# Performance work log

Measured on AMD Instinct MI355X. Metric: run time of the kernel, lower is better.

The kernel has to match this reference:

```python
import jax, jax.numpy as jnp
import numpy as np

EPS = 1e-12

def _fuzzy_laplacian_weights(theta, src, dst, num_nodes):
    # Continuous edge directions: forward (src->dst) strength cos^2(theta),
    # backward (dst->src) strength sin^2(theta); each symmetrically normalized
    # by its own weighted in/out degrees.
    c = jnp.cos(theta); s = jnp.sin(theta)
    w_f = c * c
    w_b = s * s
    def norm(w):
        deg_out = jax.ops.segment_sum(w, src, num_segments=num_nodes)
        deg_in = jax.ops.segment_sum(w, dst, num_segments=num_nodes)
        return w * jax.lax.rsqrt(deg_out[src] * deg_in[dst] + EPS)
    return norm(w_f), norm(w_b)

def setup_inputs() -> dict:
    key = jax.random.key(0)
    ks = jax.random.split(key, 12)
    N, E, D, H, O, L = 50000, 800000, 128, 128, 64, 2
    x = jax.random.normal(ks[0], (N, D), dtype=jnp.float32)
    edge_index = jax.random.randint(ks[1], (2, E), 0, N, dtype=jnp.int64)
    theta = jax.random.uniform(ks[2], (E,), dtype=jnp.float32) * (np.pi / 2)
    sc = 0.05
    Ws2d = jax.random.normal(ks[3], (L, D, H), dtype=jnp.float32) * sc
    Wd2s = jax.random.normal(ks[4], (L, D, H), dtype=jnp.float32) * sc
    Wself = jax.random.normal(ks[5], (L, D, H), dtype=jnp.float32) * sc
    bs2d = jnp.zeros((L, H), jnp.float32)
    bd2s = jnp.zeros((L, H), jnp.float32)
    bself = jnp.zeros((L, H), jnp.float32)
    W_ro = jax.random.normal(ks[6], (H, O), dtype=jnp.float32) * sc
    b_ro = jnp.zeros((O,), jnp.float32)
    return {"x": x, "edge_index": edge_index, "theta": theta,
            "Ws2d": Ws2d, "Wd2s": Wd2s, "Wself": Wself,
            "bs2d": bs2d, "bd2s": bd2s, "bself": bself,
            "W_ro": W_ro, "b_ro": b_ro}

def reference(x, edge_index, theta, Ws2d, Wd2s, Wself, bs2d, bd2s, bself, W_ro, b_ro):
    N = x.shape[0]
    src, dst = edge_index[0], edge_index[1]
    w_f, w_b = _fuzzy_laplacian_weights(theta, src, dst, N)
    L = Ws2d.shape[0]
    for i in range(L):
        xj = x[src]                               # [E, D] gather
        a_s2d = jax.ops.segment_sum(xj * w_f[:, None], dst, num_segments=N)
        a_d2s = jax.ops.segment_sum(xj * w_b[:, None], dst, num_segments=N)
        h = (a_s2d @ Ws2d[i] + bs2d[i]
             + a_d2s @ Wd2s[i] + bd2s[i]
             + x @ Wself[i] + bself[i])
        if i != L - 1:
            h = jax.nn.relu(h)
            h = h / jnp.maximum(jnp.linalg.norm(h, axis=1, keepdims=True), EPS)
        x = h
    return x @ W_ro + b_ro
```

## Files before the change

kernel.cpp:

```cpp
#include <hip/hip_runtime.h>
#include <math.h>


constexpr int D = 128;
typedef unsigned long long u64;
typedef __attribute__((ext_vector_type(8))) short bf16x8;
typedef __attribute__((ext_vector_type(4))) float f32x4;

__device__ __forceinline__ u64 pack_wc(float f) {
    return (1ULL << 44) | (u64)(f * 16777216.0f + 0.5f);
}
__device__ __forceinline__ void unpack_wc(u64 p, float& sumf, float& cnt) {
    cnt  = (float)(unsigned)(p >> 44);
    sumf = (float)(p & ((1ULL << 44) - 1)) * (1.0f / 16777216.0f);
}

__device__ __forceinline__ void split_bf16(float x, short& hi, short& lo) {
    unsigned xb = __float_as_uint(x);
    hi = (short)(xb >> 16);
    float h = __uint_as_float(xb & 0xffff0000u);
    lo = (short)(__float_as_uint(x - h) >> 16);
}

__global__ __launch_bounds__(256) void edge_wdeg_kernel(
    const float* __restrict__ theta, const int* __restrict__ src, const int* __restrict__ dst,
    u64* __restrict__ packed_out, u64* __restrict__ packed_in, int E)
{
    int e = blockIdx.x * 256 + threadIdx.x;
    if (e >= E) return;
    float c = cosf(theta[e]);
    u64 p = pack_wc(c * c);
    atomicAdd(&packed_out[src[e]], p);
    atomicAdd(&packed_in[dst[e]], p);
}

__global__ __launch_bounds__(1024) void scan_kernel(
    const u64* __restrict__ packed_in, int* __restrict__ startv, int N)
{
    __shared__ int wsum[16];
    __shared__ int carry;
    if (threadIdx.x == 0) carry = 0;
    __syncthreads();
    const int lane = threadIdx.x & 63, wid = threadIdx.x >> 6;
    for (int base = 0; base < N; base += 1024) {
        int i = base + threadIdx.x;
        int v = (i < N) ? (int)(packed_in[i] >> 44) : 0;
        int x = v;
        #pragma unroll
        for (int d = 1; d < 64; d <<= 1) {
            int t = __shfl_up(x, d);
            if (lane >= d) x += t;
        }
        if (lane == 63) wsum[wid] = x;
        __syncthreads();
        if (wid == 0) {
            int s = (lane < 16) ? wsum[lane] : 0;
            #pragma unroll
            for (int d = 1; d < 16; d <<= 1) {
                int t = __shfl_up(s, d);
                if (lane >= d) s += t;
            }
            if (lane < 16) wsum[lane] = s;
        }
        __syncthreads();
        int woff = (wid == 0) ? 0 : wsum[wid - 1];
        if (i < N) startv[i] = carry + woff + x - v;
        __syncthreads();
        if (threadIdx.x == 1023) carry += wsum[15];
        __syncthreads();
    }
}

__global__ __launch_bounds__(256) void scatter_kernel(
    const float* __restrict__ theta, const int* __restrict__ src, const int* __restrict__ dst,
    const u64* __restrict__ packed_out, const u64* __restrict__ packed_in,
    int* __restrict__ startv, int4* __restrict__ s_edge, int E)
{
    int e = blockIdx.x * 256 + threadIdx.x;
    if (e >= E) return;
    int u = src[e], v = dst[e];
    float s, c;
    sincosf(theta[e], &s, &c);
    float f = c * c, b = s * s;
    float fo, co, fi, ci;
    unpack_wc(packed_out[u], fo, co);
    unpack_wc(packed_in[v], fi, ci);
    float bo = co - fo, bi = ci - fi;
    f *= rsqrtf(fo * fi + 1e-12f);
    b *= rsqrtf(bo * bi + 1e-12f);
    int pos = atomicAdd(&startv[v], 1);
    s_edge[pos] = make_int4(u, __float_as_int(f), __float_as_int(b), 0);
}

__global__ __launch_bounds__(256) void wpack_kernel(
    const float* __restrict__ W1, const float* __restrict__ W2, const float* __restrict__ W3,
    short* __restrict__ wp)
{
    int idx = blockIdx.x * 256 + threadIdx.x;
    if (idx >= 3 * 8 * 4 * 64) return;
    int lane = idx & 63;
    int t = (idx >> 6) & 3;
    int c = (idx >> 8) & 7;
    int m = idx >> 11;
    const float* W = (m == 0) ? W1 : ((m == 1) ? W2 : W3);
    int col  = c * 16 + (lane & 15);
    int row0 = t * 32 + (lane >> 4) * 8;
    short hi[8], lo[8];
    #pragma unroll
    for (int j = 0; j < 8; ++j)
        split_bf16(W[(size_t)(row0 + j) * 128 + col], hi[j], lo[j]);
    short* dst = wp + (size_t)idx * 16;
    #pragma unroll
    for (int j = 0; j < 8; ++j) { dst[j] = hi[j]; dst[8 + j] = lo[j]; }
}

__global__ __launch_bounds__(256) void agg_x_kernel(
    const int* __restrict__ endv, const int4* __restrict__ s_edge,
    const float* __restrict__ x,
    float* __restrict__ a1, float* __restrict__ a2, int N)
{
    int v = blockIdx.x * 4 + (threadIdx.x >> 6);
    if (v >= N) return;
    int lane = threadIdx.x & 63;
    int beg = (v == 0) ? 0 : endv[v - 1];
    int end = endv[v];
    float2 s1 = make_float2(0.f, 0.f), s2 = make_float2(0.f, 0.f);
    int e = beg;
    for (; e + 1 < end; e += 2) {
        int4 E0 = s_edge[e], E1 = s_edge[e + 1];
        float f0 = __int_as_float(E0.y), b0 = __int_as_float(E0.z);
        float f1 = __int_as_float(E1.y), b1 = __int_as_float(E1.z);
        float2 x0 = reinterpret_cast<const float2*>(x + (size_t)E0.x * 128)[lane];
        float2 x1 = reinterpret_cast<const float2*>(x + (size_t)E1.x * 128)[lane];
        s1.x = fmaf(f0, x0.x, s1.x); s1.y = fmaf(f0, x0.y, s1.y);
        s2.x = fmaf(b0, x0.x, s2.x); s2.y = fmaf(b0, x0.y, s2.y);
        s1.x = fmaf(f1, x1.x, s1.x); s1.y = fmaf(f1, x1.y, s1.y);
        s2.x = fmaf(b1, x1.x, s2.x); s2.y = fmaf(b1, x1.y, s2.y);
    }
    if (e < end) {
        int4 E0 = s_edge[e];
        float f0 = __int_as_float(E0.y), b0 = __int_as_float(E0.z);
        float2 x0 = reinterpret_cast<const float2*>(x + (size_t)E0.x * 128)[lane];
        s1.x = fmaf(f0, x0.x, s1.x); s1.y = fmaf(f0, x0.y, s1.y);
        s2.x = fmaf(b0, x0.x, s2.x); s2.y = fmaf(b0, x0.y, s2.y);
    }
    reinterpret_cast<float2*>(a1 + (size_t)v * 128)[lane] = s1;
    reinterpret_cast<float2*>(a2 + (size_t)v * 128)[lane] = s2;
}

__global__ __launch_bounds__(256, 2) void matmul_fused_kernel(
    const float* __restrict__ a1, const float* __restrict__ a2,
    const float* __restrict__ xin, const short* __restrict__ wp,
    const float* __restrict__ b1, const float* __restrict__ b2, const float* __restrict__ b3,
    float* __restrict__ h, int N)
{
    const int lane = threadIdx.x & 63, wid = threadIdx.x >> 6;
    const int row0 = blockIdx.x * 64 + wid * 16;

    int arow = row0 + (lane & 15);
    if (arow >= N) arow = N - 1;
    const size_t roff = (size_t)arow * 128 + (lane >> 4) * 8;
    const float* srcs[3] = {a1, a2, xin};
    bf16x8 ahi[3][4], alo[3][4];
    #pragma unroll
    for (int m = 0; m < 3; ++m) {
        const float* rp = srcs[m] + roff;
        #pragma unroll
        for (int t = 0; t < 4; ++t) {
            float4 v0 = *reinterpret_cast<const float4*>(rp + t * 32);
            float4 v1 = *reinterpret_cast<const float4*>(rp + t * 32 + 4);
            float f[8] = {v0.x, v0.y, v0.z, v0.w, v1.x, v1.y, v1.z, v1.w};
            #pragma unroll
            for (int j = 0; j < 8; ++j) {
                short hh, ll;
                split_bf16(f[j], hh, ll);
                ahi[m][t][j] = hh;
                alo[m][t][j] = ll;
            }
        }
    }

    const int colbase = lane & 15;
    const int rbase = row0 + (lane >> 4) * 4;
    #pragma unroll
    for (int c = 0; c < 8; ++c) {
        f32x4 a = {0.f, 0.f, 0.f, 0.f};
        #pragma unroll
        for (int t = 0; t < 4; ++t) {
            #pragma unroll
            for (int m = 0; m < 3; ++m) {
                const short* bp = wp + (size_t)((m * 8 + c) * 4 + t) * 1024 + lane * 16;
                bf16x8 bhi = *reinterpret_cast<const bf16x8*>(bp);
                bf16x8 blo = *reinterpret_cast<const bf16x8*>(bp + 8);
                a = __builtin_amdgcn_mfma_f32_16x16x32_bf16(ahi[m][t], bhi, a, 0, 0, 0);
                a = __builtin_amdgcn_mfma_f32_16x16x32_bf16(ahi[m][t], blo, a, 0, 0, 0);
                a = __builtin_amdgcn_mfma_f32_16x16x32_bf16(alo[m][t], bhi, a, 0, 0, 0);
            }
        }
        int col = c * 16 + colbase;
        float bias = b1[col] + b2[col] + b3[col];
        a[0] += bias; a[1] += bias; a[2] += bias; a[3] += bias;
        #pragma unroll
        for (int r = 0; r < 4; ++r) {
            int rr = rbase + r;
            if (rr < N) h[(size_t)rr * 128 + col] = a[r];
        }
    }
}

__global__ __launch_bounds__(256) void relu_rownorm_kernel(float* __restrict__ h, int N)
{
    int row = blockIdx.x * 4 + (threadIdx.x >> 6);
    if (row >= N) return;
    int lane = threadIdx.x & 63;
    float2* p = reinterpret_cast<float2*>(h + (size_t)row * 128) + lane;
    float2 v = *p;
    v.x = fmaxf(v.x, 0.f);
    v.y = fmaxf(v.y, 0.f);
    float ss = v.x * v.x + v.y * v.y;
    #pragma unroll
    for (int m = 1; m < 64; m <<= 1) ss += __shfl_xor(ss, m);
    float sc = 1.f / fmaxf(sqrtf(ss), 1e-12f);
    v.x *= sc; v.y *= sc;
    *p = v;
}

__global__ __launch_bounds__(256) void readout_kernel(
    const float* __restrict__ x, const float* __restrict__ W,
    const float* __restrict__ bias, float* __restrict__ out, int N)
{
    __shared__ float xs[64 * 132];
    const int tid = threadIdx.x;
    const int row0 = blockIdx.x * 64;
    #pragma unroll
    for (int j = 0; j < 8; ++j) {
        int g4 = tid + j * 256;
        int r = g4 >> 5, c4 = g4 & 31;
        float4 v = make_float4(0.f, 0.f, 0.f, 0.f);
        if (row0 + r < N)
            v = reinterpret_cast<const float4*>(x + (size_t)(row0 + r) * D)[c4];
        *reinterpret_cast<float4*>(xs + r * 132 + c4 * 4) = v;
    }
    __syncthreads();

    const int cg = tid & 15;
    const int rg = tid >> 4;
    float a[4][4];
    #pragma unroll
    for (int i = 0; i < 4; ++i)
        #pragma unroll
        for (int j = 0; j < 4; ++j) a[i][j] = 0.f;

    for (int k = 0; k < 128; k += 4) {
        float4 w0 = *reinterpret_cast<const float4*>(W + (size_t)(k + 0) * 64 + cg * 4);
        float4 w1 = *reinterpret_cast<const float4*>(W + (size_t)(k + 1) * 64 + cg * 4);
        float4 w2 = *reinterpret_cast<const float4*>(W + (size_t)(k + 2) * 64 + cg * 4);
        float4 w3 = *reinterpret_cast<const float4*>(W + (size_t)(k + 3) * 64 + cg * 4);
        #pragma unroll
        for (int i = 0; i < 4; ++i) {
            float4 xv = *reinterpret_cast<const float4*>(xs + (rg * 4 + i) * 132 + k);
            a[i][0] += xv.x * w0.x + xv.y * w1.x + xv.z * w2.x + xv.w * w3.x;
            a[i][1] += xv.x * w0.y + xv.y * w1.y + xv.z * w2.y + xv.w * w3.y;
            a[i][2] += xv.x * w0.z + xv.y * w1.z + xv.z * w2.z + xv.w * w3.z;
            a[i][3] += xv.x * w0.w + xv.y * w1.w + xv.z * w2.w + xv.w * w3.w;
        }
    }
    #pragma unroll
    for (int i = 0; i < 4; ++i) {
        int r = row0 + rg * 4 + i;
        if (r < N) {
            float4 o = make_float4(a[i][0] + bias[cg * 4 + 0], a[i][1] + bias[cg * 4 + 1],
                                   a[i][2] + bias[cg * 4 + 2], a[i][3] + bias[cg * 4 + 3]);
            *reinterpret_cast<float4*>(out + (size_t)r * 64 + cg * 4) = o;
        }
    }
}

extern "C" void kernel_launch(void* const* d_in, const int* in_sizes, int n_in,
                              void* d_out, int out_size, void* d_ws, size_t ws_size,
                              hipStream_t stream)
{
    const float* x     = (const float*)d_in[0];
    const int*   ei    = (const int*)d_in[1];
    const float* theta = (const float*)d_in[2];
    const float* Ws2d  = (const float*)d_in[3];
    const float* Wd2s  = (const float*)d_in[4];
    const float* Wself = (const float*)d_in[5];
    const float* bs2d  = (const float*)d_in[6];
    const float* bd2s  = (const float*)d_in[7];
    const float* bself = (const float*)d_in[8];
    const float* W_ro  = (const float*)d_in[9];
    const float* b_ro  = (const float*)d_in[10];
    float* out = (float*)d_out;

    const int N = in_sizes[0] / D;
    const int E = in_sizes[2];
    const int L = in_sizes[3] / (D * D);

    const int* src = ei;
    const int* dst = ei + E;

    u64*  packed_out = (u64*)d_ws;
    u64*  packed_in  = packed_out + N;
    int*  startv     = (int*)(packed_in + N);
    int4* s_edge     = (int4*)(startv + N);
    short* wpack     = (short*)(s_edge + E);
    float* a1   = (float*)(wpack + (size_t)L * 98304);
    float* a2   = a1 + (size_t)N * D;
    float* accA = a2 + (size_t)N * D;
    float* accB = accA + (size_t)N * D;

    hipMemsetAsync(packed_out, 0, (size_t)2 * N * sizeof(u64), stream);
    edge_wdeg_kernel<<<(E + 255) / 256, 256, 0, stream>>>(
        theta, src, dst, packed_out, packed_in, E);
    scan_kernel<<<1, 1024, 0, stream>>>(packed_in, startv, N);
    scatter_kernel<<<(E + 255) / 256, 256, 0, stream>>>(
        theta, src, dst, packed_out, packed_in, startv, s_edge, E);
    for (int i = 0; i < L; ++i)
        wpack_kernel<<<(6144 + 255) / 256, 256, 0, stream>>>(
            Ws2d + (size_t)i * D * D, Wd2s + (size_t)i * D * D, Wself + (size_t)i * D * D,
            wpack + (size_t)i * 98304);

    const float* xin = x;
    float* accs[2] = {accA, accB};
    for (int i = 0; i < L; ++i) {
        float* acc = accs[i & 1];
        agg_x_kernel<<<(N + 3) / 4, 256, 0, stream>>>(
            startv, s_edge, xin, a1, a2, N);
        matmul_fused_kernel<<<(N + 63) / 64, 256, 0, stream>>>(
            a1, a2, xin, wpack + (size_t)i * 98304,
            bs2d + (size_t)i * D, bd2s + (size_t)i * D, bself + (size_t)i * D,
            acc, N);
        if (i != L - 1)
            relu_rownorm_kernel<<<(N + 3) / 4, 256, 0, stream>>>(acc, N);
        xin = acc;
    }
    readout_kernel<<<(N + 63) / 64, 256, 0, stream>>>(xin, W_ro, b_ro, out, N);
}
```

Measured before the change: 537.4 us.

## Fuse relu-rownorm into matmul, MFMA readout, unroll aggregation, two-per-thread scan

The ReLU and row L2-normalisation are folded into the matmul epilogue. The 128-column row norm is reduced across the 16 lanes that hold a row, which removes a separate kernel's full read and write of the hidden matrix. The scalar-FMA readout kernel becomes an MFMA kernel using a bf16 hi/lo split of W_ro, packed once by a new small kernel. The aggregation loop is unrolled to four edges to keep more gathers in flight, and the scan handles two elements per thread to halve its iterations. The cost is more register pressure in the matmul, which now keeps all eight output tiles live.

```diff
diff --git a/kernel.cpp b/kernel.cpp
--- a/kernel.cpp
+++ b/kernel.cpp
@@ -42,10 +42,13 @@
     if (threadIdx.x == 0) carry = 0;
     __syncthreads();
     const int lane = threadIdx.x & 63, wid = threadIdx.x >> 6;
-    for (int base = 0; base < N; base += 1024) {
-        int i = base + threadIdx.x;
-        int v = (i < N) ? (int)(packed_in[i] >> 44) : 0;
-        int x = v;
+    for (int base = 0; base < N; base += 2048) {
+        int i0 = base + threadIdx.x * 2;
+        int i1 = i0 + 1;
+        int v0 = (i0 < N) ? (int)(packed_in[i0] >> 44) : 0;
+        int v1 = (i1 < N) ? (int)(packed_in[i1] >> 44) : 0;
+        int pair = v0 + v1;
+        int x = pair;
         #pragma unroll
         for (int d = 1; d < 64; d <<= 1) {
             int t = __shfl_up(x, d);
@@ -64,7 +67,9 @@
         }
         __syncthreads();
         int woff = (wid == 0) ? 0 : wsum[wid - 1];
-        if (i < N) startv[i] = carry + woff + x - v;
+        int excl = carry + woff + x - pair;
+        if (i0 < N) startv[i0] = excl;
+        if (i1 < N) startv[i1] = excl + v0;
         __syncthreads();
         if (threadIdx.x == 1023) carry += wsum[15];
         __syncthreads();
@@ -114,6 +119,25 @@
     for (int j = 0; j < 8; ++j) { dst[j] = hi[j]; dst[8 + j] = lo[j]; }
 }
 
+__global__ __launch_bounds__(256) void wpack_ro_kernel(
+    const float* __restrict__ W, short* __restrict__ wp)
+{
+    int idx = blockIdx.x * 256 + threadIdx.x;
+    if (idx >= 4 * 4 * 64) return;
+    int lane = idx & 63;
+    int t = (idx >> 6) & 3;
+    int c = idx >> 8;
+    int col  = c * 16 + (lane & 15);
+    int row0 = t * 32 + (lane >> 4) * 8;
+    short hi[8], lo[8];
+    #pragma unroll
+    for (int j = 0; j < 8; ++j)
+        split_bf16(W[(size_t)(row0 + j) * 64 + col], hi[j], lo[j]);
+    short* dst = wp + (size_t)idx * 16;
+    #pragma unroll
+    for (int j = 0; j < 8; ++j) { dst[j] = hi[j]; dst[8 + j] = lo[j]; }
+}
+
 __global__ __launch_bounds__(256) void agg_x_kernel(
     const int* __restrict__ endv, const int4* __restrict__ s_edge,
     const float* __restrict__ x,
@@ -126,18 +150,26 @@
     int end = endv[v];
     float2 s1 = make_float2(0.f, 0.f), s2 = make_float2(0.f, 0.f);
     int e = beg;
-    for (; e + 1 < end; e += 2) {
-        int4 E0 = s_edge[e], E1 = s_edge[e + 1];
+    for (; e + 3 < end; e += 4) {
+        int4 E0 = s_edge[e], E1 = s_edge[e + 1], E2 = s_edge[e + 2], E3 = s_edge[e + 3];
+        float2 x0 = reinterpret_cast<const float2*>(x + (size_t)E0.x * 128)[lane];
+        float2 x1 = reinterpret_cast<const float2*>(x + (size_t)E1.x * 128)[lane];
+        float2 x2 = reinterpret_cast<const float2*>(x + (size_t)E2.x * 128)[lane];
+        float2 x3 = reinterpret_cast<const float2*>(x + (size_t)E3.x * 128)[lane];
         float f0 = __int_as_float(E0.y), b0 = __int_as_float(E0.z);
         float f1 = __int_as_float(E1.y), b1 = __int_as_float(E1.z);
-        float2 x0 = reinterpret_cast<const float2*>(x + (size_t)E0.x * 128)[lane];
-        float2 x1 = reinterpret_cast<const float2*>(x + (size_t)E1.x * 128)[lane];
+        float f2 = __int_as_float(E2.y), b2 = __int_as_float(E2.z);
+        float f3 = __int_as_float(E3.y), b3 = __int_as_float(E3.z);
         s1.x = fmaf(f0, x0.x, s1.x); s1.y = fmaf(f0, x0.y, s1.y);
         s2.x = fmaf(b0, x0.x, s2.x); s2.y = fmaf(b0, x0.y, s2.y);
         s1.x = fmaf(f1, x1.x, s1.x); s1.y = fmaf(f1, x1.y, s1.y);
         s2.x = fmaf(b1, x1.x, s2.x); s2.y = fmaf(b1, x1.y, s2.y);
-    }
-    if (e < end) {
+        s1.x = fmaf(f2, x2.x, s1.x); s1.y = fmaf(f2, x2.y, s1.y);
+        s2.x = fmaf(b2, x2.x, s2.x); s2.y = fmaf(b2, x2.y, s2.y);
+        s1.x = fmaf(f3, x3.x, s1.x); s1.y = fmaf(f3, x3.y, s1.y);
+        s2.x = fmaf(b3, x3.x, s2.x); s2.y = fmaf(b3, x3.y, s2.y);
+    }
+    for (; e < end; ++e) {
         int4 E0 = s_edge[e];
         float f0 = __int_as_float(E0.y), b0 = __int_as_float(E0.z);
         float2 x0 = reinterpret_cast<const float2*>(x + (size_t)E0.x * 128)[lane];
@@ -148,6 +180,7 @@
     reinterpret_cast<float2*>(a2 + (size_t)v * 128)[lane] = s2;
 }
 
+template <bool NORM>
 __global__ __launch_bounds__(256, 2) void matmul_fused_kernel(
     const float* __restrict__ a1, const float* __restrict__ a2,
     const float* __restrict__ xin, const short* __restrict__ wp,
@@ -182,6 +215,7 @@
 
     const int colbase = lane & 15;
     const int rbase = row0 + (lane >> 4) * 4;
+    f32x4 acc[8];
     #pragma unroll
     for (int c = 0; c < 8; ++c) {
         f32x4 a = {0.f, 0.f, 0.f, 0.f};
@@ -200,78 +234,97 @@
         int col = c * 16 + colbase;
         float bias = b1[col] + b2[col] + b3[col];
         a[0] += bias; a[1] += bias; a[2] += bias; a[3] += bias;
+        acc[c] = a;
+    }
+
+    if (NORM) {
+        #pragma unroll
+        for (int c = 0; c < 8; ++c) {
+            acc[c][0] = fmaxf(acc[c][0], 0.f);
+            acc[c][1] = fmaxf(acc[c][1], 0.f);
+            acc[c][2] = fmaxf(acc[c][2], 0.f);
+            acc[c][3] = fmaxf(acc[c][3], 0.f);
+        }
+        float ss[4] = {0.f, 0.f, 0.f, 0.f};
+        #pragma unroll
+        for (int c = 0; c < 8; ++c) {
+            ss[0] = fmaf(acc[c][0], acc[c][0], ss[0]);
+            ss[1] = fmaf(acc[c][1], acc[c][1], ss[1]);
+            ss[2] = fmaf(acc[c][2], acc[c][2], ss[2]);
+            ss[3] = fmaf(acc[c][3], acc[c][3], ss[3]);
+        }
+        #pragma unroll
+        for (int r = 0; r < 4; ++r) {
+            #pragma unroll
+            for (int m = 1; m < 16; m <<= 1) ss[r] += __shfl_xor(ss[r], m);
+        }
+        float sc[4];
+        #pragma unroll
+        for (int r = 0; r < 4; ++r) sc[r] = 1.f / fmaxf(sqrtf(ss[r]), 1e-12f);
+        #pragma unroll
+        for (int c = 0; c < 8; ++c) {
+            acc[c][0] *= sc[0]; acc[c][1] *= sc[1];
+            acc[c][2] *= sc[2]; acc[c][3] *= sc[3];
+        }
+    }
+
+    #pragma unroll
+    for (int c = 0; c < 8; ++c) {
+        int col = c * 16 + colbase;
         #pragma unroll
         for (int r = 0; r < 4; ++r) {
             int rr = rbase + r;
-            if (rr < N) h[(size_t)rr * 128 + col] = a[r];
-        }
-    }
-}
-
-__global__ __launch_bounds__(256) void relu_rownorm_kernel(float* __restrict__ h, int N)
-{
-    int row = blockIdx.x * 4 + (threadIdx.x >> 6);
-    if (row >= N) return;
-    int lane = threadIdx.x & 63;
-    float2* p = reinterpret_cast<float2*>(h + (size_t)row * 128) + lane;
-    float2 v = *p;
-    v.x = fmaxf(v.x, 0.f);
-    v.y = fmaxf(v.y, 0.f);
-    float ss = v.x * v.x + v.y * v.y;
-    #pragma unroll
-    for (int m = 1; m < 64; m <<= 1) ss += __shfl_xor(ss, m);
-    float sc = 1.f / fmaxf(sqrtf(ss), 1e-12f);
-    v.x *= sc; v.y *= sc;
-    *p = v;
-}
-
-__global__ __launch_bounds__(256) void readout_kernel(
-    const float* __restrict__ x, const float* __restrict__ W,
+            if (rr < N) h[(size_t)rr * 128 + col] = acc[c][r];
+        }
+    }
+}
+
+__global__ __launch_bounds__(256, 2) void readout_mfma_kernel(
+    const float* __restrict__ xin, const short* __restrict__ wp,
     const float* __restrict__ bias, float* __restrict__ out, int N)
 {
-    __shared__ float xs[64 * 132];
-    const int tid = threadIdx.x;
-    const int row0 = blockIdx.x * 64;
-    #pragma unroll
-    for (int j = 0; j < 8; ++j) {
-        int g4 = tid + j * 256;
-        int r = g4 >> 5, c4 = g4 & 31;
-        float4 v = make_float4(0.f, 0.f, 0.f, 0.f);
-        if (row0 + r < N)
-            v = reinterpret_cast<const float4*>(x + (size_t)(row0 + r) * D)[c4];
-        *reinterpret_cast<float4*>(xs + r * 132 + c4 * 4) = v;
-    }
-    __syncthreads();
-
-    const int cg = tid & 15;
-    const int rg = tid >> 4;
-    float a[4][4];
-    #pragma unroll
-    for (int i = 0; i < 4; ++i)
-        #pragma unroll
-        for (int j = 0; j < 4; ++j) a[i][j] = 0.f;
-
-    for (int k = 0; k < 128; k += 4) {
-        float4 w0 = *reinterpret_cast<const float4*>(W + (size_t)(k + 0) * 64 + cg * 4);
-        float4 w1 = *reinterpret_cast<const float4*>(W + (size_t)(k + 1) * 64 + cg * 4);
-        float4 w2 = *reinterpret_cast<const float4*>(W + (size_t)(k + 2) * 64 + cg * 4);
-        float4 w3 = *reinterpret_cast<const float4*>(W + (size_t)(k + 3) * 64 + cg * 4);
-        #pragma unroll
-        for (int i = 0; i < 4; ++i) {
-            float4 xv = *reinterpret_cast<const float4*>(xs + (rg * 4 + i) * 132 + k);
-            a[i][0] += xv.x * w0.x + xv.y * w1.x + xv.z * w2.x + xv.w * w3.x;
-            a[i][1] += xv.x * w0.y + xv.y * w1.y + xv.z * w2.y + xv.w * w3.y;
-            a[i][2] += xv.x * w0.z + xv.y * w1.z + xv.z * w2.z + xv.w * w3.z;
-            a[i][3] += xv.x * w0.w + xv.y * w1.w + xv.z * w2.w + xv.w * w3.w;
-        }
-    }
-    #pragma unroll
-    for (int i = 0; i < 4; ++i) {
-        int r = row0 + rg * 4 + i;
-        if (r < N) {
-            float4 o = make_float4(a[i][0] + bias[cg * 4 + 0], a[i][1] + bias[cg * 4 + 1],
-                                   a[i][2] + bias[cg * 4 + 2], a[i][3] + bias[cg * 4 + 3]);
-            *reinterpret_cast<float4*>(out + (size_t)r * 64 + cg * 4) = o;
+    const int lane = threadIdx.x & 63, wid = threadIdx.x >> 6;
+    const int row0 = blockIdx.x * 64 + wid * 16;
+
+    int arow = row0 + (lane & 15);
+    if (arow >= N) arow = N - 1;
+    const float* rp = xin + (size_t)arow * 128 + (lane >> 4) * 8;
+    bf16x8 ahi[4], alo[4];
+    #pragma unroll
+    for (int t = 0; t < 4; ++t) {
+        float4 v0 = *reinterpret_cast<const float4*>(rp + t * 32);
+        float4 v1 = *reinterpret_cast<const float4*>(rp + t * 32 + 4);
+        float f[8] = {v0.x, v0.y, v0.z, v0.w, v1.x, v1.y, v1.z, v1.w};
+        #pragma unroll
+        for (int j = 0; j < 8; ++j) {
+            short hh, ll;
+            split_bf16(f[j], hh, ll);
+            ahi[t][j] = hh;
+            alo[t][j] = ll;
+        }
+    }
+
+    const int colbase = lane & 15;
+    const int rbase = row0 + (lane >> 4) * 4;
+    #pragma unroll
+    for (int c = 0; c < 4; ++c) {
+        f32x4 a = {0.f, 0.f, 0.f, 0.f};
+        #pragma unroll
+        for (int t = 0; t < 4; ++t) {
+            const short* bp = wp + (size_t)((c * 4 + t) * 64 + lane) * 16;
+            bf16x8 bhi = *reinterpret_cast<const bf16x8*>(bp);
+            bf16x8 blo = *reinterpret_cast<const bf16x8*>(bp + 8);
+            a = __builtin_amdgcn_mfma_f32_16x16x32_bf16(ahi[t], bhi, a, 0, 0, 0);
+            a = __builtin_amdgcn_mfma_f32_16x16x32_bf16(ahi[t], blo, a, 0, 0, 0);
+            a = __builtin_amdgcn_mfma_f32_16x16x32_bf16(alo[t], bhi, a, 0, 0, 0);
+        }
+        int col = c * 16 + colbase;
+        float bv = bias[col];
+        a[0] += bv; a[1] += bv; a[2] += bv; a[3] += bv;
+        #pragma unroll
+        for (int r = 0; r < 4; ++r) {
+            int rr = rbase + r;
+            if (rr < N) out[(size_t)rr * 64 + col] = a[r];
         }
     }
 }
@@ -305,7 +358,8 @@
     int*  startv     = (int*)(packed_in + N);
     int4* s_edge     = (int4*)(startv + N);
     short* wpack     = (short*)(s_edge + E);
-    float* a1   = (float*)(wpack + (size_t)L * 98304);
+    short* wpack_ro  = wpack + (size_t)L * 98304;
+    float* a1   = (float*)(wpack_ro + 16384);
     float* a2   = a1 + (size_t)N * D;
     float* accA = a2 + (size_t)N * D;
     float* accB = accA + (size_t)N * D;
@@ -320,6 +374,7 @@
         wpack_kernel<<<(6144 + 255) / 256, 256, 0, stream>>>(
             Ws2d + (size_t)i * D * D, Wd2s + (size_t)i * D * D, Wself + (size_t)i * D * D,
             wpack + (size_t)i * 98304);
+    wpack_ro_kernel<<<4, 256, 0, stream>>>(W_ro, wpack_ro);
 
     const float* xin = x;
     float* accs[2] = {accA, accB};
@@ -327,13 +382,17 @@
         float* acc = accs[i & 1];
         agg_x_kernel<<<(N + 3) / 4, 256, 0, stream>>>(
             startv, s_edge, xin, a1, a2, N);
-        matmul_fused_kernel<<<(N + 63) / 64, 256, 0, stream>>>(
-            a1, a2, xin, wpack + (size_t)i * 98304,
-            bs2d + (size_t)i * D, bd2s + (size_t)i * D, bself + (size_t)i * D,
-            acc, N);
         if (i != L - 1)
-            relu_rownorm_kernel<<<(N + 3) / 4, 256, 0, stream>>>(acc, N);
+            matmul_fused_kernel<true><<<(N + 63) / 64, 256, 0, stream>>>(
+                a1, a2, xin, wpack + (size_t)i * 98304,
+                bs2d + (size_t)i * D, bd2s + (size_t)i * D, bself + (size_t)i * D,
+                acc, N);
+        else
+            matmul_fused_kernel<false><<<(N + 63) / 64, 256, 0, stream>>>(
+                a1, a2, xin, wpack + (size_t)i * 98304,
+                bs2d + (size_t)i * D, bd2s + (size_t)i * D, bself + (size_t)i * D,
+                acc, N);
         xin = acc;
     }
-    readout_kernel<<<(N + 63) / 64, 256, 0, stream>>>(xin, W_ro, b_ro, out, N);
-}
+    readout_mfma_kernel<<<(N + 63) / 64, 256, 0, stream>>>(xin, wpack_ro, b_ro, out, N);
+}
```

Measured after the change: 498.2 us. -7.3%, faster.
